# Performance work log

Hardware: AMD Instinct MI355X
Metric: run time of the kernel (lower is better)

## Reference

```python
import jax, jax.numpy as jnp
import numpy as np

B, S, I, H = 64, 2048, 128, 256


def setup_inputs() -> dict:
    key = jax.random.key(0)
    ks = jax.random.split(key, 14)
    std = 1.0 / np.sqrt(H)
    def mat(k, shape):
        # xavier-normal-ish init (exact distribution irrelevant for correctness)
        fan_in, fan_out = shape
        s = np.sqrt(2.0 / (fan_in + fan_out))
        return jax.random.normal(k, shape, dtype=jnp.float32) * s
    def vec(k):
        return jax.random.uniform(k, (H,), dtype=jnp.float32, minval=-std, maxval=std)
    return {
        "x": jax.random.normal(ks[0], (B, S, I), dtype=jnp.float32),
        "U_f": mat(ks[1], (I, H)), "W_f": mat(ks[2], (H, H)), "b_f": vec(ks[3]),
        "U_i": mat(ks[4], (I, H)), "W_i": mat(ks[5], (H, H)), "b_i": vec(ks[6]),
        "U_o": mat(ks[7], (I, H)), "W_o": mat(ks[8], (H, H)), "b_o": vec(ks[9]),
        "U_c": mat(ks[10], (I, H)), "W_c": mat(ks[11], (H, H)), "b_c": vec(ks[12]),
    }


def _lstm(x, U_f, W_f, b_f, U_i, W_i, b_i, U_o, W_o, b_o, U_c, W_c, b_c):
    batch, seq, _ = x.shape
    hid = W_f.shape[0]
    # Fuse the 4 input projections into one GEMM over the whole sequence (same math).
    U = jnp.concatenate([U_f, U_i, U_o, U_c], axis=1)           # [I, 4H]
    W = jnp.concatenate([W_f, W_i, W_o, W_c], axis=1)           # [H, 4H]
    b = jnp.concatenate([b_f, b_i, b_o, b_c], axis=0)           # [4H]
    xg = jnp.einsum('bsi,ig->sbg', x, U) + b                    # [S, B, 4H]

    def step(carry, xg_t):
        h, c = carry
        g = xg_t + h @ W                                         # [B, 4H]
        f_t = jax.nn.sigmoid(g[:, 0 * hid:1 * hid])
        i_t = jax.nn.sigmoid(g[:, 1 * hid:2 * hid])
        o_t = jax.nn.sigmoid(g[:, 2 * hid:3 * hid])
        # NOTE: source uses sigmoid (not tanh) for the candidate cell
        c_tilde = jax.nn.sigmoid(g[:, 3 * hid:4 * hid])
        c_new = f_t * c + i_t * c_tilde
        h_new = o_t * jnp.tanh(c_new)
        return (h_new, c_new), h_new

    h0 = jnp.zeros((batch, hid), dtype=x.dtype)
    c0 = jnp.zeros((batch, hid), dtype=x.dtype)
    (h_T, c_T), hs = jax.lax.scan(step, (h0, c0), xg)
    hidden_seq = jnp.transpose(hs, (1, 0, 2))                    # [B, S, H]
    return hidden_seq, (h_T, c_T)


def reference(x, U_f, W_f, b_f, U_i, W_i, b_i, U_o, W_o, b_o, U_c, W_c, b_c):
    return _lstm(x, U_f, W_f, b_f, U_i, W_i, b_i, U_o, W_o, b_o, U_c, W_c, b_c)
```

## Files before the change

### kernel.cpp

```cpp
#include <hip/hip_runtime.h>
#include <stdint.h>

typedef unsigned short ushort_t;
typedef unsigned int uint32;

#define SEQ   2048
#define BATCH 64
#define INDIM 128
#define HID   256
#define NGRP  4
#define NWGG  16
#define HSZ   (BATCH*SEQ*HID)

typedef __attribute__((ext_vector_type(8))) short short8;
typedef __attribute__((ext_vector_type(4))) float float4_t;
typedef __attribute__((ext_vector_type(2))) uint32 uint2_t;

__device__ __forceinline__ ushort_t f2bf(float f) {
  uint32 u = __builtin_bit_cast(uint32, f);
  u += 0x7FFFu + ((u >> 16) & 1u);
  return (ushort_t)(u >> 16);
}
__device__ __forceinline__ float fast_sigmoid(float x) {
  return 1.0f / (1.0f + __expf(-x));
}
__device__ __forceinline__ float fast_tanh(float x) {
  return 1.0f - 2.0f / (__expf(2.0f * x) + 1.0f);
}
template<int CTRL>
__device__ __forceinline__ float bcast_quad(float v) {
  int r = __builtin_amdgcn_mov_dpp(__builtin_bit_cast(int, v), CTRL, 0xF, 0xF, true);
  return __builtin_bit_cast(float, r);
}

__device__ __forceinline__ void load16_bypass(short8& d, const ushort_t* p) {
  asm volatile("global_load_dwordx4 %0, %1, off sc0 sc1"
               : "=v"(d) : "v"(p) : "memory");
}
__device__ __forceinline__ void store8_bypass(uint2_t* p, uint2_t v) {
  asm volatile("global_store_dwordx2 %0, %1, off sc0 sc1"
               :: "v"(p), "v"(v) : "memory");
}
__device__ __forceinline__ void store_dword_bypass(uint32* p, uint32 v) {
  asm volatile("global_store_dword %0, %1, off sc0 sc1"
               :: "v"(p), "v"(v) : "memory");
}
__device__ __forceinline__ uint32 load_dword_bypass(const uint32* p) {
  uint32 v;
  asm volatile("global_load_dword %0, %1, off sc0 sc1\n\ts_waitcnt vmcnt(0)"
               : "=v"(v) : "v"(p) : "memory");
  return v;
}
__device__ __forceinline__ void wait8(short8* c) {
  asm volatile("s_waitcnt vmcnt(0)"
               : "+v"(c[0]), "+v"(c[1]), "+v"(c[2]), "+v"(c[3]),
                 "+v"(c[4]), "+v"(c[5]), "+v"(c[6]), "+v"(c[7])
               :: "memory");
}
__device__ __forceinline__ void drain_vm() {
  asm volatile("s_waitcnt vmcnt(0)" ::: "memory");
}

__global__ void pack_init(const float* __restrict__ x,
                          const float* __restrict__ Wf, const float* __restrict__ Wi,
                          const float* __restrict__ Wo, const float* __restrict__ Wc,
                          const float* __restrict__ Uf, const float* __restrict__ Ui,
                          const float* __restrict__ Uo, const float* __restrict__ Uc,
                          const float* __restrict__ bf_, const float* __restrict__ bi_,
                          const float* __restrict__ bo_, const float* __restrict__ bc_,
                          ushort_t* __restrict__ BM2, float* __restrict__ bp2,
                          ushort_t* __restrict__ xbf, uint32* __restrict__ flags) {
  int idx = blockIdx.x * 256 + threadIdx.x;
  {
    int e = idx & 7, lane = (idx >> 3) & 63, q = (idx >> 9) & 3,
        grp = (idx >> 11) & 3, t = idx >> 13;
    if (t < SEQ) {
      int row = grp * 16 + (lane & 15);
      int k = q * 32 + (lane >> 4) * 8 + e;
      xbf[idx] = f2bf(x[(row * SEQ + t) * INDIM + k]);
    }
  }
  if (idx < 64 * 12 * 512) {
    int e = idx & 7, lane = (idx >> 3) & 63;
    int kf = (idx >> 9) % 12, jw = (idx >> 9) / 12;
    int w = jw & 3, j = jw >> 2;
    int llo = lane & 15, lhi = lane >> 4;
    int n = j * 16 + w * 4 + (llo >> 2);
    int g = llo & 3;
    int k = kf * 32 + lhi * 8 + e;
    const float* W4[4] = {Wf, Wi, Wo, Wc};
    const float* U4[4] = {Uf, Ui, Uo, Uc};
    float v = (k < HID) ? W4[g][k * HID + n] : U4[g][(k - HID) * HID + n];
    BM2[idx] = f2bf(v);
  }
  if (idx < 1024) {
    int llo = idx & 15, jw = idx >> 4;
    int w = jw & 3, j = jw >> 2;
    int n = j * 16 + w * 4 + (llo >> 2);
    int g = llo & 3;
    const float* B4[4] = {bf_, bi_, bo_, bc_};
    bp2[idx] = B4[g][n];
  }
  if (idx < NGRP * 64) flags[idx] = 0;
}

__global__ __launch_bounds__(256, 1) void lstm_seq(
    const ushort_t* __restrict__ xbf, const ushort_t* __restrict__ BM2,
    const float* __restrict__ bp2, uint2_t* hpub, uint32* flags,
    float* __restrict__ out)
{
  const int i    = blockIdx.x & 3;
  const int j    = blockIdx.x >> 2;
  const int tid  = threadIdx.x;
  const int wave = tid >> 6;
  const int lane = tid & 63;
  const int lhi  = lane >> 4;
  const int llo  = lane & 15;
  const int Lr   = lane & 3;
  const int Lq   = (lane >> 2) & 3;

  short8 bfrag[12];
  {
    const ushort_t* bsrc = BM2 + (size_t)((j * 4 + wave) * 12) * 512 + lane * 8;
#pragma unroll
    for (int kf = 0; kf < 12; ++kf)
      bfrag[kf] = *(const short8*)(bsrc + kf * 512);
  }
  const float bias = bp2[(j * 4 + wave) * 16 + llo];

  float c_reg[4] = {0.f, 0.f, 0.f, 0.f};
  const int sown = j * 4 + wave;
  uint32* myflag = &flags[(i << 6) + sown];
  const uint32* pollp = &flags[(i << 6) + lane];

  short8 xq[4];
  {
    const ushort_t* xs = xbf + (size_t)i * 2048 + lane * 8;
#pragma unroll
    for (int q = 0; q < 4; ++q) xq[q] = *(const short8*)(xs + q * 512);
  }

  for (int t = 0; t < SEQ; ++t) {
    float4_t acc = {bias, bias, bias, bias};
#pragma unroll
    for (int q = 0; q < 4; ++q)
      acc = __builtin_amdgcn_mfma_f32_16x16x32_bf16(xq[q], bfrag[8 + q], acc, 0, 0, 0);

    if (t > 0) {
      uint32 v = load_dword_bypass(pollp);
      while (__any((int)(v < (uint32)t))) {
        __builtin_amdgcn_s_sleep(2);
        v = load_dword_bypass(pollp);
      }
      const ushort_t* hb = (const ushort_t*)
          (hpub + (size_t)(i * 2 + ((t - 1) & 1)) * 1024);
      short8 hf[8];
#pragma unroll
      for (int kf = 0; kf < 8; ++kf)
        load16_bypass(hf[kf], hb + (((kf * 4 + lhi) * 16 + llo) * 2) * 4);
      wait8(hf);
#pragma unroll
      for (int kf = 0; kf < 8; ++kf)
        acc = __builtin_amdgcn_mfma_f32_16x16x32_bf16(hf[kf], bfrag[kf], acc, 0, 0, 0);
    }

    float hv[4], cnv[4];
#pragma unroll
    for (int r = 0; r < 4; ++r) {
      float s  = fast_sigmoid(acc[r]);
      float fv = bcast_quad<0x00>(s);
      float iv = bcast_quad<0x55>(s);
      float ov = bcast_quad<0xAA>(s);
      float cv = bcast_quad<0xFF>(s);
      float cn = fv * c_reg[r] + iv * cv;
      c_reg[r] = cn;
      cnv[r] = cn;
      hv[r] = ov * fast_tanh(cn);
    }

    float o0 = 0.f, o1 = 0.f, o2 = 0.f, o3 = 0.f;
#pragma unroll
    for (int r = 0; r < 4; ++r) {
      int sl = Lq * 16;
      float a = __shfl(hv[r], sl + 0);
      float b = __shfl(hv[r], sl + 4);
      float c2 = __shfl(hv[r], sl + 8);
      float d = __shfl(hv[r], sl + 12);
      if (Lr == r) { o0 = a; o1 = b; o2 = c2; o3 = d; }
    }

    if (t < SEQ - 1) {
      if (lane < 16) {
        uint32 u0 = (uint32)f2bf(o0) | ((uint32)f2bf(o1) << 16);
        uint32 u1 = (uint32)f2bf(o2) | ((uint32)f2bf(o3) << 16);
        uint2_t pv = {u0, u1};
        store8_bypass(hpub + (size_t)(i * 2 + (t & 1)) * 1024 +
                      (sown >> 1) * 32 + lane * 2 + (sown & 1), pv);
      }
      drain_vm();
      if (lane == 0)
        store_dword_bypass(myflag, (uint32)(t + 1));
      if (lane < 16) {
        float4_t ov4 = {o0, o1, o2, o3};
        *(float4_t*)(out + ((size_t)(16 * i + lane) * SEQ + t) * HID +
                     j * 16 + wave * 4) = ov4;
      }
      const ushort_t* xs = xbf + (size_t)((t + 1) * 4 + i) * 2048 + lane * 8;
#pragma unroll
      for (int q = 0; q < 4; ++q) xq[q] = *(const short8*)(xs + q * 512);
    } else {
      if (lane < 16) {
        float4_t ov4 = {o0, o1, o2, o3};
        *(float4_t*)(out + ((size_t)(16 * i + lane) * SEQ + t) * HID +
                     j * 16 + wave * 4) = ov4;
        *(float4_t*)(out + HSZ + (size_t)(16 * i + lane) * HID +
                     j * 16 + wave * 4) = ov4;
      }
      float p0 = 0.f, p1 = 0.f, p2 = 0.f, p3 = 0.f;
#pragma unroll
      for (int r = 0; r < 4; ++r) {
        int sl = Lq * 16;
        float a = __shfl(cnv[r], sl + 0);
        float b = __shfl(cnv[r], sl + 4);
        float c2 = __shfl(cnv[r], sl + 8);
        float d = __shfl(cnv[r], sl + 12);
        if (Lr == r) { p0 = a; p1 = b; p2 = c2; p3 = d; }
      }
      if (lane < 16) {
        float4_t cv4 = {p0, p1, p2, p3};
        *(float4_t*)(out + HSZ + BATCH * HID + (size_t)(16 * i + lane) * HID +
                     j * 16 + wave * 4) = cv4;
      }
    }
  }
}

extern "C" void kernel_launch(void* const* d_in, const int* in_sizes, int n_in,
                              void* d_out, int out_size, void* d_ws, size_t ws_size,
                              hipStream_t stream) {
  const float* xp  = (const float*)d_in[0];
  const float* Uf  = (const float*)d_in[1];
  const float* Wf  = (const float*)d_in[2];
  const float* bf_ = (const float*)d_in[3];
  const float* Ui  = (const float*)d_in[4];
  const float* Wi  = (const float*)d_in[5];
  const float* bi_ = (const float*)d_in[6];
  const float* Uo  = (const float*)d_in[7];
  const float* Wo  = (const float*)d_in[8];
  const float* bo_ = (const float*)d_in[9];
  const float* Uc  = (const float*)d_in[10];
  const float* Wc  = (const float*)d_in[11];
  const float* bc_ = (const float*)d_in[12];

  char* ws = (char*)d_ws;
  ushort_t* BM2   = (ushort_t*)(ws);
  float*    bp2   = (float*)(ws + 786432);
  uint2_t*  hpub  = (uint2_t*)(ws + 790528);
  uint32*   flags = (uint32*)(ws + 856064);
  ushort_t* xbf   = (ushort_t*)(ws + 1048576);
  float*    out   = (float*)d_out;

  pack_init<<<65536, 256, 0, stream>>>(xp, Wf, Wi, Wo, Wc, Uf, Ui, Uo, Uc,
                                       bf_, bi_, bo_, bc_, BM2, bp2, xbf, flags);
  lstm_seq<<<NGRP * NWGG, 256, 0, stream>>>(xbf, BM2, bp2, hpub, flags, out);
}
```

Before: 5.121 ms.

## Pipeline flag polling, split MFMA accumulators, and drop shuffle transpose for direct stores

Replaces the blocking spin-poll with two in-flight poll loads that alternate, so a fresh flag read is already pending while the previous one is checked, and the exit test is now wave-wide __all. Splits the recurrent h@W MFMA chain into two independent accumulators to shorten the dependent chain. Removes the 16 cross-lane shuffles used to gather h values, having every lane write its own element with scalar bf16 and fp32 stores instead of 16 lanes writing vectors. This cuts per-step latency on the serial critical path, at the cost of more, narrower global stores.

```diff
diff --git a/kernel.cpp b/kernel.cpp
--- a/kernel.cpp
+++ b/kernel.cpp
@@ -37,19 +37,23 @@
   asm volatile("global_load_dwordx4 %0, %1, off sc0 sc1"
                : "=v"(d) : "v"(p) : "memory");
 }
-__device__ __forceinline__ void store8_bypass(uint2_t* p, uint2_t v) {
-  asm volatile("global_store_dwordx2 %0, %1, off sc0 sc1"
+__device__ __forceinline__ void store_short_bypass(ushort_t* p, uint32 v) {
+  asm volatile("global_store_short %0, %1, off sc0 sc1"
                :: "v"(p), "v"(v) : "memory");
 }
 __device__ __forceinline__ void store_dword_bypass(uint32* p, uint32 v) {
   asm volatile("global_store_dword %0, %1, off sc0 sc1"
                :: "v"(p), "v"(v) : "memory");
 }
-__device__ __forceinline__ uint32 load_dword_bypass(const uint32* p) {
-  uint32 v;
-  asm volatile("global_load_dword %0, %1, off sc0 sc1\n\ts_waitcnt vmcnt(0)"
+__device__ __forceinline__ void issue_poll(uint32& v, const uint32* p) {
+  asm volatile("global_load_dword %0, %1, off sc0 sc1"
                : "=v"(v) : "v"(p) : "memory");
-  return v;
+}
+__device__ __forceinline__ void wait_vm1(uint32& v) {
+  asm volatile("s_waitcnt vmcnt(1)" : "+v"(v) :: "memory");
+}
+__device__ __forceinline__ void drain_tied2(uint32& a, uint32& b) {
+  asm volatile("s_waitcnt vmcnt(0)" : "+v"(a), "+v"(b) :: "memory");
 }
 __device__ __forceinline__ void wait8(short8* c) {
   asm volatile("s_waitcnt vmcnt(0)"
@@ -117,7 +121,8 @@
   const int lhi  = lane >> 4;
   const int llo  = lane & 15;
   const int Lr   = lane & 3;
-  const int Lq   = (lane >> 2) & 3;
+  const int csub = llo >> 2;
+  const int row  = lhi * 4 + Lr;
 
   short8 bfrag[12];
   {
@@ -130,6 +135,7 @@
 
   float c_reg[4] = {0.f, 0.f, 0.f, 0.f};
   const int sown = j * 4 + wave;
+  const int colg = sown * 4 + csub;
   uint32* myflag = &flags[(i << 6) + sown];
   const uint32* pollp = &flags[(i << 6) + lane];
 
@@ -145,13 +151,23 @@
 #pragma unroll
     for (int q = 0; q < 4; ++q)
       acc = __builtin_amdgcn_mfma_f32_16x16x32_bf16(xq[q], bfrag[8 + q], acc, 0, 0, 0);
+    float4_t accA = {0.f, 0.f, 0.f, 0.f};
+    float4_t accB = {0.f, 0.f, 0.f, 0.f};
 
     if (t > 0) {
-      uint32 v = load_dword_bypass(pollp);
-      while (__any((int)(v < (uint32)t))) {
-        __builtin_amdgcn_s_sleep(2);
-        v = load_dword_bypass(pollp);
+      const uint32 want = (uint32)t;
+      uint32 va, vb;
+      issue_poll(va, pollp);
+      issue_poll(vb, pollp);
+      for (;;) {
+        wait_vm1(va);
+        if (__all((int)(va >= want))) break;
+        issue_poll(va, pollp);
+        wait_vm1(vb);
+        if (__all((int)(vb >= want))) break;
+        issue_poll(vb, pollp);
       }
+      drain_tied2(va, vb);
       const ushort_t* hb = (const ushort_t*)
           (hpub + (size_t)(i * 2 + ((t - 1) & 1)) * 1024);
       short8 hf[8];
@@ -160,77 +176,47 @@
         load16_bypass(hf[kf], hb + (((kf * 4 + lhi) * 16 + llo) * 2) * 4);
       wait8(hf);
 #pragma unroll
-      for (int kf = 0; kf < 8; ++kf)
-        acc = __builtin_amdgcn_mfma_f32_16x16x32_bf16(hf[kf], bfrag[kf], acc, 0, 0, 0);
-    }
-
-    float hv[4], cnv[4];
+      for (int kf = 0; kf < 4; ++kf) {
+        accA = __builtin_amdgcn_mfma_f32_16x16x32_bf16(hf[2 * kf],     bfrag[2 * kf],     accA, 0, 0, 0);
+        accB = __builtin_amdgcn_mfma_f32_16x16x32_bf16(hf[2 * kf + 1], bfrag[2 * kf + 1], accB, 0, 0, 0);
+      }
+    }
+
+    float hv0, hv1, hv2, hv3;
 #pragma unroll
     for (int r = 0; r < 4; ++r) {
-      float s  = fast_sigmoid(acc[r]);
+      float s  = fast_sigmoid(acc[r] + accA[r] + accB[r]);
       float fv = bcast_quad<0x00>(s);
       float iv = bcast_quad<0x55>(s);
       float ov = bcast_quad<0xAA>(s);
       float cv = bcast_quad<0xFF>(s);
       float cn = fv * c_reg[r] + iv * cv;
       c_reg[r] = cn;
-      cnv[r] = cn;
-      hv[r] = ov * fast_tanh(cn);
-    }
-
-    float o0 = 0.f, o1 = 0.f, o2 = 0.f, o3 = 0.f;
-#pragma unroll
-    for (int r = 0; r < 4; ++r) {
-      int sl = Lq * 16;
-      float a = __shfl(hv[r], sl + 0);
-      float b = __shfl(hv[r], sl + 4);
-      float c2 = __shfl(hv[r], sl + 8);
-      float d = __shfl(hv[r], sl + 12);
-      if (Lr == r) { o0 = a; o1 = b; o2 = c2; o3 = d; }
-    }
+      float h  = ov * fast_tanh(cn);
+      if      (r == 0) hv0 = h;
+      else if (r == 1) hv1 = h;
+      else if (r == 2) hv2 = h;
+      else             hv3 = h;
+    }
+    float val = (Lr == 0) ? hv0 : (Lr == 1) ? hv1 : (Lr == 2) ? hv2 : hv3;
 
     if (t < SEQ - 1) {
-      if (lane < 16) {
-        uint32 u0 = (uint32)f2bf(o0) | ((uint32)f2bf(o1) << 16);
-        uint32 u1 = (uint32)f2bf(o2) | ((uint32)f2bf(o3) << 16);
-        uint2_t pv = {u0, u1};
-        store8_bypass(hpub + (size_t)(i * 2 + (t & 1)) * 1024 +
-                      (sown >> 1) * 32 + lane * 2 + (sown & 1), pv);
-      }
+      ushort_t* hbo = (ushort_t*)(hpub + (size_t)(i * 2 + (t & 1)) * 1024);
+      store_short_bypass(hbo + ((sown >> 1) * 32 + row * 2 + (sown & 1)) * 4 + csub,
+                         (uint32)f2bf(val));
       drain_vm();
       if (lane == 0)
         store_dword_bypass(myflag, (uint32)(t + 1));
-      if (lane < 16) {
-        float4_t ov4 = {o0, o1, o2, o3};
-        *(float4_t*)(out + ((size_t)(16 * i + lane) * SEQ + t) * HID +
-                     j * 16 + wave * 4) = ov4;
-      }
+      out[((size_t)(16 * i + row) * SEQ + t) * HID + colg] = val;
       const ushort_t* xs = xbf + (size_t)((t + 1) * 4 + i) * 2048 + lane * 8;
 #pragma unroll
       for (int q = 0; q < 4; ++q) xq[q] = *(const short8*)(xs + q * 512);
     } else {
-      if (lane < 16) {
-        float4_t ov4 = {o0, o1, o2, o3};
-        *(float4_t*)(out + ((size_t)(16 * i + lane) * SEQ + t) * HID +
-                     j * 16 + wave * 4) = ov4;
-        *(float4_t*)(out + HSZ + (size_t)(16 * i + lane) * HID +
-                     j * 16 + wave * 4) = ov4;
-      }
-      float p0 = 0.f, p1 = 0.f, p2 = 0.f, p3 = 0.f;
-#pragma unroll
-      for (int r = 0; r < 4; ++r) {
-        int sl = Lq * 16;
-        float a = __shfl(cnv[r], sl + 0);
-        float b = __shfl(cnv[r], sl + 4);
-        float c2 = __shfl(cnv[r], sl + 8);
-        float d = __shfl(cnv[r], sl + 12);
-        if (Lr == r) { p0 = a; p1 = b; p2 = c2; p3 = d; }
-      }
-      if (lane < 16) {
-        float4_t cv4 = {p0, p1, p2, p3};
-        *(float4_t*)(out + HSZ + BATCH * HID + (size_t)(16 * i + lane) * HID +
-                     j * 16 + wave * 4) = cv4;
-      }
+      out[((size_t)(16 * i + row) * SEQ + t) * HID + colg] = val;
+      out[HSZ + (size_t)(16 * i + row) * HID + colg] = val;
+      float cva = (Lr == 0) ? c_reg[0] : (Lr == 1) ? c_reg[1]
+                : (Lr == 2) ? c_reg[2] : c_reg[3];
+      out[HSZ + BATCH * HID + (size_t)(16 * i + row) * HID + colg] = cva;
     }
   }
 }
```

New measurement: 4.636 ms. 1.1x faster.
